# Kernel optimization log

Hardware: AMD Instinct MI355X
Metric: run time of the kernel (lower is better)

Reference implementation:

```python
import jax, jax.numpy as jnp
import numpy as np

CHANNELS = 256

def setup_inputs() -> dict:
    key = jax.random.key(0)
    ks = jax.random.split(key, 7)
    B, C, N = 4, CHANNELS, 4096
    scale = 1.0 / np.sqrt(C)
    x = jax.random.normal(ks[0], (B, C, N), dtype=jnp.float32)
    Wq = jax.random.normal(ks[1], (C, C), dtype=jnp.float32) * scale
    bq = jax.random.normal(ks[2], (C,), dtype=jnp.float32) * 0.01
    Wk = jax.random.normal(ks[3], (C, C), dtype=jnp.float32) * scale
    bk = jax.random.normal(ks[4], (C,), dtype=jnp.float32) * 0.01
    Wv = jax.random.normal(ks[5], (C, C), dtype=jnp.float32) * scale
    bv = jax.random.normal(ks[6], (C,), dtype=jnp.float32) * 0.01
    return {"x": x, "Wq": Wq, "bq": bq, "Wk": Wk, "bk": bk, "Wv": Wv, "bv": bv}

def reference(x, Wq, bq, Wk, bk, Wv, bv):
    # x: [B, C, N]; 1x1 Conv1d == channel-mixing matmul
    C = x.shape[1]
    Q = jnp.einsum('oc,bcn->bon', Wq, x) + bq[None, :, None]   # [B, C, N]
    K = jnp.einsum('oc,bcn->bon', Wk, x) + bk[None, :, None]   # [B, C, N]
    V = jnp.einsum('oc,bcn->bon', Wv, x) + bv[None, :, None]   # [B, C, N]
    # attn[b, i, j] = softmax_j( Q[:, i]^T K[:, j] / sqrt(C) )
    scores = jnp.einsum('bci,bcj->bij', Q, K) / jnp.sqrt(jnp.asarray(C, x.dtype))
    attn = jax.nn.softmax(scores, axis=-1)                     # [B, N, N]
    context = jnp.einsum('bij,bcj->bci', attn, V)              # [B, C, N]
    return x + context
```

## Files before the change

### kernel.cpp

```cpp
#include <hip/hip_runtime.h>
#include <stdint.h>

#define B_ 4
#define C_ 256
#define N_ 4096
#define JS 4

typedef unsigned short u16;
typedef __attribute__((ext_vector_type(4))) float f32x4;
typedef __attribute__((ext_vector_type(16))) float f32x16;
typedef __attribute__((ext_vector_type(8))) short bf16x8;
typedef __attribute__((ext_vector_type(4))) int i32x4;

__device__ __forceinline__ u16 f2bf(float f) {
    uint32_t u = __float_as_uint(f);
    u += 0x7fffu + ((u >> 16) & 1u);
    return (u16)(u >> 16);
}
__device__ __forceinline__ float bf2f(u16 v) {
    uint32_t u = ((uint32_t)v) << 16;
    return __uint_as_float(u);
}
__device__ __forceinline__ uint32_t pkbf(float a, float b) {
    uint32_t ua = __float_as_uint(a) + 0x8000u;
    uint32_t ub = __float_as_uint(b) + 0x8000u;
    return (ua >> 16) | (ub & 0xffff0000u);
}

#if defined(__has_builtin)
#if __has_builtin(__builtin_amdgcn_global_load_lds)
#define HAVE_GLL 1
#endif
#endif

#ifdef HAVE_GLL
__device__ __forceinline__ void g2l16(const u16* g, u16* lbase, int lane) {
    (void)lane;
    __builtin_amdgcn_global_load_lds(
        (__attribute__((address_space(1))) void*)(uintptr_t)g,
        (__attribute__((address_space(3))) void*)lbase, 16, 0, 0);
}
#else
__device__ __forceinline__ void g2l16(const u16* g, u16* lbase, int lane) {
    *(i32x4*)(lbase + lane * 8) = *(const i32x4*)g;
}
#endif

__global__ __launch_bounds__(256) void wconv_kernel(
    const float* __restrict__ Wq, const float* __restrict__ Wk,
    const float* __restrict__ Wv, u16* __restrict__ Wb) {
    int id = blockIdx.x * 256 + threadIdx.x;
    const float* src = (id < 65536) ? Wq : ((id < 131072) ? Wk : Wv);
    Wb[id] = f2bf(src[id & 65535]);
}

__global__ __launch_bounds__(256, 2) void qkv_kernel(
    const float* __restrict__ x, const u16* __restrict__ Wb,
    const float* __restrict__ bq, const float* __restrict__ bk,
    const float* __restrict__ bv,
    u16* __restrict__ Qt, u16* __restrict__ Kt, u16* __restrict__ Vt) {
    const int XTS = 264;
    __shared__ __align__(16) u16 xT[32 * XTS];

    int blk = blockIdx.x;
    int n0  = (blk & 127) << 5;
    int b   = blk >> 7;
    int tid = threadIdx.x;
    int lane = tid & 63;
    int w = tid >> 6;
    int l31 = lane & 31;
    int h = lane >> 5;

    {
        int c0 = tid >> 3;
        int nq = (tid & 7) << 2;
        const float* xb = x + ((size_t)b * C_ + c0) * N_ + n0 + nq;
        #pragma unroll
        for (int p = 0; p < 8; ++p) {
            f32x4 v = *(const f32x4*)(xb + (size_t)32 * N_ * p);
            int cc = c0 + 32 * p;
            xT[(nq + 0) * XTS + cc] = f2bf(v[0]);
            xT[(nq + 1) * XTS + cc] = f2bf(v[1]);
            xT[(nq + 2) * XTS + cc] = f2bf(v[2]);
            xT[(nq + 3) * XTS + cc] = f2bf(v[3]);
        }
    }
    __syncthreads();

    bf16x8 xf[16];
    #pragma unroll
    for (int ks = 0; ks < 16; ++ks)
        xf[ks] = *(const bf16x8*)(&xT[l31 * XTS + 16 * ks + 8 * h]);

    #pragma unroll
    for (int mat = 0; mat < 2; ++mat) {
        const u16* W = Wb + mat * 65536;
        const float* bias = mat ? bk : bq;
        u16* dst = mat ? Kt : Qt;
        f32x16 acc0, acc1;
        #pragma unroll
        for (int r = 0; r < 16; ++r) { acc0[r] = 0.f; acc1[r] = 0.f; }
        const u16* wr0 = W + (size_t)(64 * w + l31) * 256 + 8 * h;
        const u16* wr1 = W + (size_t)(64 * w + 32 + l31) * 256 + 8 * h;
        #pragma unroll
        for (int ks = 0; ks < 16; ++ks) {
            bf16x8 wf0 = *(const bf16x8*)(wr0 + 16 * ks);
            bf16x8 wf1 = *(const bf16x8*)(wr1 + 16 * ks);
            acc0 = __builtin_amdgcn_mfma_f32_32x32x16_bf16(xf[ks], wf0, acc0, 0, 0, 0);
            acc1 = __builtin_amdgcn_mfma_f32_32x32x16_bf16(xf[ks], wf1, acc1, 0, 0, 0);
        }
        #pragma unroll
        for (int ot = 0; ot < 2; ++ot) {
            const f32x16& a = ot ? acc1 : acc0;
            int o = 64 * w + 32 * ot + l31;
            float bo = bias[o];
            #pragma unroll
            for (int g = 0; g < 4; ++g)
                #pragma unroll
                for (int r = 0; r < 4; ++r) {
                    int n = 8 * g + 4 * h + r;
                    int oc = mat ? ((((o >> 3) ^ n) << 3) | (o & 7)) : o;
                    dst[((size_t)b * N_ + n0 + n) * C_ + oc] = f2bf(a[4 * g + r] + bo);
                }
        }
    }

    {
        const u16* W = Wb + 2 * 65536;
        f32x16 acc0, acc1;
        #pragma unroll
        for (int r = 0; r < 16; ++r) { acc0[r] = 0.f; acc1[r] = 0.f; }
        const u16* wr0 = W + (size_t)(64 * w + l31) * 256 + 8 * h;
        const u16* wr1 = W + (size_t)(64 * w + 32 + l31) * 256 + 8 * h;
        #pragma unroll
        for (int ks = 0; ks < 16; ++ks) {
            bf16x8 wf0 = *(const bf16x8*)(wr0 + 16 * ks);
            bf16x8 wf1 = *(const bf16x8*)(wr1 + 16 * ks);
            acc0 = __builtin_amdgcn_mfma_f32_32x32x16_bf16(wf0, xf[ks], acc0, 0, 0, 0);
            acc1 = __builtin_amdgcn_mfma_f32_32x32x16_bf16(wf1, xf[ks], acc1, 0, 0, 0);
        }
        int nj = n0 + l31;
        int tb = nj & ~63;
        int local = nj & 63;
        #pragma unroll
        for (int mt = 0; mt < 2; ++mt) {
            const f32x16& a = mt ? acc1 : acc0;
            #pragma unroll
            for (int g = 0; g < 4; ++g)
                #pragma unroll
                for (int r = 0; r < 4; ++r) {
                    int o = 64 * w + 32 * mt + 8 * g + 4 * h + r;
                    int njs = tb | ((((local >> 3) ^ (o & 7)) << 3) | (local & 7));
                    Vt[((size_t)b * C_ + o) * N_ + njs] = f2bf(a[4 * g + r] + bv[o]);
                }
        }
    }
}

__device__ __forceinline__ void stage64(const u16* Kb, const u16* Vb, int j0,
                                        u16* ksd, u16* vsd, int w, int lane) {
    const u16* kg = Kb + (size_t)(j0 + 8 * w) * C_ + lane * 8;
    u16* kdb = ksd + 8 * w * 256;
    #pragma unroll
    for (int rr = 0; rr < 4; ++rr)
        g2l16(kg + rr * 512, kdb + rr * 512, lane);
    const u16* vg = Vb + (size_t)(32 * w + (lane >> 3)) * N_ + j0 + (lane & 7) * 8;
    u16* vdb = vsd + 32 * w * 64;
    #pragma unroll
    for (int rr = 0; rr < 4; ++rr)
        g2l16(vg + (size_t)8 * rr * N_, vdb + rr * 512, lane);
}

__global__ __launch_bounds__(512, 2) void attn_kernel(
    const u16* __restrict__ Qt, const u16* __restrict__ Kt,
    const u16* __restrict__ Vt, u16* __restrict__ Op,
    float* __restrict__ lArr) {
    __shared__ __align__(16) u16 Ksh[2 * 64 * 256];
    __shared__ __align__(16) u16 Vsh[2 * 256 * 64];

    int blk = blockIdx.x;
    int it = blk & 15;
    int b  = (blk >> 4) & 3;
    int s  = blk >> 6;
    int i0 = it << 8;
    int tid = threadIdx.x;
    int lane = tid & 63;
    int w = tid >> 6;
    int l31 = lane & 31;
    int h = lane >> 5;

    bf16x8 qf[16];
    {
        const u16* qrow = Qt + ((size_t)b * N_ + i0 + 32 * w + l31) * C_ + 8 * h;
        #pragma unroll
        for (int ks = 0; ks < 16; ++ks) qf[ks] = *(const bf16x8*)(qrow + 16 * ks);
    }

    f32x16 oacc[8];
    #pragma unroll
    for (int mt = 0; mt < 8; ++mt)
        #pragma unroll
        for (int r = 0; r < 16; ++r) oacc[mt][r] = 0.f;
    float l_run = 0.f;

    const float sconst = 0.0625f * 1.44269504088896340736f;
    const u16* Kb = Kt + (size_t)b * N_ * C_;
    const u16* Vb = Vt + (size_t)b * C_ * N_;
    int jbase = s * (N_ / JS);

    stage64(Kb, Vb, jbase, Ksh, Vsh, w, lane);
    __syncthreads();

    for (int jt = 0; jt < N_ / (64 * JS); ++jt) {
        int cur = jt & 1;
        const u16* ks_ = Ksh + cur * 64 * 256;
        const u16* vs_ = Vsh + cur * 256 * 64;

        if (jt + 1 < N_ / (64 * JS))
            stage64(Kb, Vb, jbase + (jt + 1) * 64,
                    Ksh + (cur ^ 1) * 64 * 256, Vsh + (cur ^ 1) * 256 * 64, w, lane);

        f32x16 st0, st1;
        #pragma unroll
        for (int r = 0; r < 16; ++r) { st0[r] = 0.f; st1[r] = 0.f; }
        #pragma unroll
        for (int ks = 0; ks < 16; ++ks) {
            int kc = ((2 * ks + h) ^ l31) << 3;
            bf16x8 kf0 = *(const bf16x8*)(ks_ + l31 * 256 + kc);
            bf16x8 kf1 = *(const bf16x8*)(ks_ + (32 + l31) * 256 + kc);
            st0 = __builtin_amdgcn_mfma_f32_32x32x16_bf16(kf0, qf[ks], st0, 0, 0, 0);
            st1 = __builtin_amdgcn_mfma_f32_32x32x16_bf16(kf1, qf[ks], st1, 0, 0, 0);
        }

        float psum = 0.f;
        uint32_t pd[16];
        #pragma unroll
        for (int u = 0; u < 8; ++u) {
            const f32x16& stv = (u < 4) ? st0 : st1;
            int g = u & 3;
            #pragma unroll
            for (int d = 0; d < 2; ++d) {
                float p0 = exp2f(stv[4 * g + 2 * d + 0] * sconst);
                float p1 = exp2f(stv[4 * g + 2 * d + 1] * sconst);
                psum += p0 + p1;
                pd[u * 2 + d] = pkbf(p0, p1);
            }
        }
        psum += __shfl_xor(psum, 32);
        l_run += psum;

        bf16x8 pf[4];
        #pragma unroll
        for (int ks2 = 0; ks2 < 4; ++ks2) {
            uint32_t oA0 = pd[4 * ks2 + 0], oA1 = pd[4 * ks2 + 1];
            uint32_t oB0 = pd[4 * ks2 + 2], oB1 = pd[4 * ks2 + 3];
            uint32_t sn0 = h ? oA0 : oB0, sn1 = h ? oA1 : oB1;
            uint32_t rc0 = (uint32_t)__shfl_xor((int)sn0, 32);
            uint32_t rc1 = (uint32_t)__shfl_xor((int)sn1, 32);
            uint32_t ow0 = h ? oB0 : oA0, ow1 = h ? oB1 : oA1;
            i32x4 fr;
            fr[0] = (int)(h ? rc0 : ow0);
            fr[1] = (int)(h ? rc1 : ow1);
            fr[2] = (int)(h ? ow0 : rc0);
            fr[3] = (int)(h ? ow1 : rc1);
            pf[ks2] = *(bf16x8*)&fr;
        }

        #pragma unroll
        for (int ks2 = 0; ks2 < 4; ++ks2) {
            int vc = ((2 * ks2 + h) ^ (l31 & 7)) << 3;
            #pragma unroll
            for (int mt = 0; mt < 8; ++mt) {
                bf16x8 vf = *(const bf16x8*)(vs_ + (32 * mt + l31) * 64 + vc);
                oacc[mt] = __builtin_amdgcn_mfma_f32_32x32x16_bf16(vf, pf[ks2], oacc[mt], 0, 0, 0);
            }
        }
        __syncthreads();
    }

    int i = i0 + 32 * w + l31;
    u16* ob = Op + ((size_t)(s * B_ + b) * C_) * N_ + i;
    #pragma unroll
    for (int mt = 0; mt < 8; ++mt)
        #pragma unroll
        for (int g = 0; g < 4; ++g)
            #pragma unroll
            for (int r = 0; r < 4; ++r) {
                int c = 32 * mt + 8 * g + r + 4 * h;
                ob[(size_t)c * N_] = f2bf(oacc[mt][4 * g + r]);
            }
    if (h == 0) lArr[(size_t)(s * B_ + b) * N_ + i] = l_run;
}

__global__ __launch_bounds__(256) void merge_kernel(
    const float* __restrict__ x, const u16* __restrict__ Op,
    const float* __restrict__ lArr, float* __restrict__ out) {
    int blk = blockIdx.x;
    int ch = blk & 1;
    int ib = (blk >> 1) & 63;
    int b  = blk >> 7;
    int i  = ib * 64 + (threadIdx.x & 63);
    int csub = threadIdx.x >> 6;

    float L = 0.f;
    #pragma unroll
    for (int s = 0; s < JS; ++s) L += lArr[(size_t)(s * B_ + b) * N_ + i];
    float rL = 1.0f / L;

    for (int cc = 0; cc < 32; ++cc) {
        int c = ch * 128 + csub * 32 + cc;
        size_t xi = ((size_t)b * C_ + c) * N_ + i;
        float acc = 0.f;
        #pragma unroll
        for (int s = 0; s < JS; ++s)
            acc += bf2f(Op[((size_t)(s * B_ + b) * C_ + c) * N_ + i]);
        out[xi] = fmaf(acc, rL, x[xi]);
    }
}

extern "C" void kernel_launch(void* const* d_in, const int* in_sizes, int n_in,
                              void* d_out, int out_size, void* d_ws, size_t ws_size,
                              hipStream_t stream) {
    const float* x  = (const float*)d_in[0];
    const float* Wq = (const float*)d_in[1];
    const float* bq = (const float*)d_in[2];
    const float* Wk = (const float*)d_in[3];
    const float* bk = (const float*)d_in[4];
    const float* Wv = (const float*)d_in[5];
    const float* bv = (const float*)d_in[6];
    float* out = (float*)d_out;

    u16* Wb = (u16*)d_ws;
    u16* Qt = Wb + 3 * 65536;
    u16* Kt = Qt + (size_t)B_ * N_ * C_;
    u16* Vt = Kt + (size_t)B_ * N_ * C_;
    u16* Op = Vt + (size_t)B_ * N_ * C_;
    float* lArr = (float*)(Op + (size_t)JS * B_ * C_ * N_);

    wconv_kernel<<<768, 256, 0, stream>>>(Wq, Wk, Wv, Wb);
    qkv_kernel<<<512, 256, 0, stream>>>(x, Wb, bq, bk, bv, Qt, Kt, Vt);
    attn_kernel<<<256, 512, 0, stream>>>(Qt, Kt, Vt, Op, lArr);
    merge_kernel<<<512, 256, 0, stream>>>(x, Op, lArr, out);
}
```

Baseline: 205.3 us.

## Vectorize merge kernel, use native exp2, raise wave priority around MFMA loops

Rewrites the merge kernel so each thread handles 8 contiguous positions over 2 channels using 16-byte bf16 and float4 loads and stores. The reciprocal row sums are computed once per block into shared memory, and the grid is doubled to 1024 blocks. The attention kernel swaps exp2f for the raw hardware exp2 builtin, dropping range handling, and brackets both MFMA loops with s_setprio so matrix-issuing waves get scheduling priority. The exp2 change trades a little accuracy for fewer instructions, and the priority hints may or may not help interleaving.

```diff
diff --git a/kernel.cpp b/kernel.cpp
--- a/kernel.cpp
+++ b/kernel.cpp
@@ -25,6 +25,18 @@
     uint32_t ua = __float_as_uint(a) + 0x8000u;
     uint32_t ub = __float_as_uint(b) + 0x8000u;
     return (ua >> 16) | (ub & 0xffff0000u);
+}
+
+__device__ __forceinline__ float fexp2(float x) {
+#if defined(__has_builtin)
+#if __has_builtin(__builtin_amdgcn_exp2f)
+    return __builtin_amdgcn_exp2f(x);
+#else
+    return exp2f(x);
+#endif
+#else
+    return exp2f(x);
+#endif
 }
 
 #if defined(__has_builtin)
@@ -223,6 +235,7 @@
         f32x16 st0, st1;
         #pragma unroll
         for (int r = 0; r < 16; ++r) { st0[r] = 0.f; st1[r] = 0.f; }
+        __builtin_amdgcn_s_setprio(1);
         #pragma unroll
         for (int ks = 0; ks < 16; ++ks) {
             int kc = ((2 * ks + h) ^ l31) << 3;
@@ -231,6 +244,7 @@
             st0 = __builtin_amdgcn_mfma_f32_32x32x16_bf16(kf0, qf[ks], st0, 0, 0, 0);
             st1 = __builtin_amdgcn_mfma_f32_32x32x16_bf16(kf1, qf[ks], st1, 0, 0, 0);
         }
+        __builtin_amdgcn_s_setprio(0);
 
         float psum = 0.f;
         uint32_t pd[16];
@@ -240,8 +254,8 @@
             int g = u & 3;
             #pragma unroll
             for (int d = 0; d < 2; ++d) {
-                float p0 = exp2f(stv[4 * g + 2 * d + 0] * sconst);
-                float p1 = exp2f(stv[4 * g + 2 * d + 1] * sconst);
+                float p0 = fexp2(stv[4 * g + 2 * d + 0] * sconst);
+                float p1 = fexp2(stv[4 * g + 2 * d + 1] * sconst);
                 psum += p0 + p1;
                 pd[u * 2 + d] = pkbf(p0, p1);
             }
@@ -266,6 +280,7 @@
             pf[ks2] = *(bf16x8*)&fr;
         }
 
+        __builtin_amdgcn_s_setprio(1);
         #pragma unroll
         for (int ks2 = 0; ks2 < 4; ++ks2) {
             int vc = ((2 * ks2 + h) ^ (l31 & 7)) << 3;
@@ -275,6 +290,7 @@
                 oacc[mt] = __builtin_amdgcn_mfma_f32_32x32x16_bf16(vf, pf[ks2], oacc[mt], 0, 0, 0);
             }
         }
+        __builtin_amdgcn_s_setprio(0);
         __syncthreads();
     }
 
@@ -295,26 +311,49 @@
 __global__ __launch_bounds__(256) void merge_kernel(
     const float* __restrict__ x, const u16* __restrict__ Op,
     const float* __restrict__ lArr, float* __restrict__ out) {
+    __shared__ float rLs[64];
     int blk = blockIdx.x;
-    int ch = blk & 1;
-    int ib = (blk >> 1) & 63;
-    int b  = blk >> 7;
-    int i  = ib * 64 + (threadIdx.x & 63);
-    int csub = threadIdx.x >> 6;
-
-    float L = 0.f;
-    #pragma unroll
-    for (int s = 0; s < JS; ++s) L += lArr[(size_t)(s * B_ + b) * N_ + i];
-    float rL = 1.0f / L;
-
-    for (int cc = 0; cc < 32; ++cc) {
-        int c = ch * 128 + csub * 32 + cc;
-        size_t xi = ((size_t)b * C_ + c) * N_ + i;
-        float acc = 0.f;
-        #pragma unroll
-        for (int s = 0; s < JS; ++s)
-            acc += bf2f(Op[((size_t)(s * B_ + b) * C_ + c) * N_ + i]);
-        out[xi] = fmaf(acc, rL, x[xi]);
+    int cg = blk & 3;
+    int ic = (blk >> 2) & 63;
+    int b  = blk >> 8;
+    int i0 = ic << 6;
+    int tid = threadIdx.x;
+
+    if (tid < 64) {
+        float L = 0.f;
+        #pragma unroll
+        for (int s = 0; s < JS; ++s) L += lArr[(size_t)(s * B_ + b) * N_ + i0 + tid];
+        rLs[tid] = 1.0f / L;
+    }
+    __syncthreads();
+
+    int i8 = (tid & 7) << 3;
+    int c  = (cg << 6) + ((tid >> 3) << 1);
+    f32x4 rl0 = *(const f32x4*)&rLs[i8];
+    f32x4 rl1 = *(const f32x4*)&rLs[i8 + 4];
+
+    #pragma unroll
+    for (int cc = 0; cc < 2; ++cc) {
+        size_t xoff = ((size_t)b * C_ + c + cc) * N_ + i0 + i8;
+        float acc[8];
+        #pragma unroll
+        for (int e = 0; e < 8; ++e) acc[e] = 0.f;
+        #pragma unroll
+        for (int s = 0; s < JS; ++s) {
+            bf16x8 o = *(const bf16x8*)&Op[((size_t)(s * B_ + b) * C_ + c + cc) * N_ + i0 + i8];
+            #pragma unroll
+            for (int e = 0; e < 8; ++e) acc[e] += bf2f((u16)o[e]);
+        }
+        f32x4 xv0 = *(const f32x4*)&x[xoff];
+        f32x4 xv1 = *(const f32x4*)&x[xoff + 4];
+        f32x4 o0, o1;
+        #pragma unroll
+        for (int e = 0; e < 4; ++e) {
+            o0[e] = fmaf(acc[e], rl0[e], xv0[e]);
+            o1[e] = fmaf(acc[e + 4], rl1[e], xv1[e]);
+        }
+        *(f32x4*)&out[xoff] = o0;
+        *(f32x4*)&out[xoff + 4] = o1;
     }
 }
 
@@ -340,5 +379,5 @@
     wconv_kernel<<<768, 256, 0, stream>>>(Wq, Wk, Wv, Wb);
     qkv_kernel<<<512, 256, 0, stream>>>(x, Wb, bq, bk, bv, Qt, Kt, Vt);
     attn_kernel<<<256, 512, 0, stream>>>(Qt, Kt, Vt, Op, lArr);
-    merge_kernel<<<512, 256, 0, stream>>>(x, Op, lArr, out);
-}
+    merge_kernel<<<1024, 256, 0, stream>>>(x, Op, lArr, out);
+}
```

New measurement: 194.9 us. -5.1%, faster.
